# Kernel tuning notes

Measured on AMD Instinct MI355X. Metric: run time of the kernel, lower is better.

## Reference

```python
import jax, jax.numpy as jnp
import numpy as np


def setup_inputs() -> dict:
    key = jax.random.key(0)
    k1, k2, k3 = jax.random.split(key, 3)
    x = jax.random.normal(k1, (64, 64, 128, 128), dtype=jnp.float32)
    weight = jax.random.normal(k2, (256, 64, 3, 3), dtype=jnp.float32)
    bias = jax.random.normal(k3, (256,), dtype=jnp.float32)
    return {"x": x, "weight": weight, "bias": bias}


def reference(x, weight, bias):
    # Conv2d, stride 1, no padding (VALID), NCHW / OIHW layout
    y = jax.lax.conv_general_dilated(
        x, weight,
        window_strides=(1, 1),
        padding='VALID',
        dimension_numbers=('NCHW', 'OIHW', 'NCHW'),
    )
    y = y + bias[None, :, None, None]  # [B, C_out, H_out, W_out]
    # tanh-approximate GELU (matches the Triton kernel's formula)
    y = jax.nn.gelu(y, approximate=True)
    # global average pool over spatial dims -> [B, C_out]
    return jnp.mean(y, axis=(2, 3))
```

## Files before the change

kernel.cpp:

```cpp
#include <hip/hip_runtime.h>


typedef __attribute__((ext_vector_type(8))) short short8;
typedef __attribute__((ext_vector_type(4))) float floatx4;
typedef __attribute__((ext_vector_type(4))) unsigned int uintx4;
typedef __attribute__((ext_vector_type(2))) unsigned int uintx2;

#define HO 126
#define CIP 72

__device__ __forceinline__ unsigned int f2bf(float f) {
    unsigned int u = __float_as_uint(f);
    return (u + 0x7FFFu + ((u >> 16) & 1u)) >> 16;
}

__device__ __forceinline__ float gelu_t(float y) {
    float p = __builtin_fmaf(0.044715f, y * y, 1.0f);
    float z2 = -2.3022084f * y * p;
    float e = exp2f(z2);
    return y * __builtin_amdgcn_rcpf(1.0f + e);
}

__global__ __launch_bounds__(256)
void prep_kernel(const float* __restrict__ wgt, float* __restrict__ out,
                 unsigned short* __restrict__ wb2) {
    int g = blockIdx.x * 256 + threadIdx.x;
    if (g < 64 * 256) out[g] = 0.f;
    if (g < 147456) {
        int j    = g & 7;
        int lane = (g >> 3) & 63;
        int fc   = g >> 9;
        int cog  = fc & 15;
        int half = (fc >> 4) & 1;
        int tap  = fc >> 5;
        int li = lane & 15, quad = lane >> 4;
        int co = cog * 16 + li;
        int ci = half * 32 + quad * 8 + j;
        wb2[g] = (unsigned short)f2bf(wgt[(co * 64 + ci) * 9 + tap]);
    }
}

__global__ __launch_bounds__(512, 4)
void conv_kernel(const float* __restrict__ x, const float* __restrict__ bias,
                 const unsigned short* __restrict__ wb2, float* __restrict__ out) {
    __shared__ unsigned short xs[3][130][CIP];

    const int bx = blockIdx.x;
    const int n = bx / HO;
    const int h = bx % HO;
    const int tid  = threadIdx.x;
    const int lane = tid & 63;
    const int wave = tid >> 6;
    const int li   = lane & 15;
    const int quad = lane >> 4;
    const int sc = wave & 3;
    const int sp = wave >> 2;
    const int coBase  = sc * 64;
    const int pixBase = sp * 64;

    {
        const int col = tid & 127;
        const int g   = tid >> 7;
        const float* xg = x + (size_t)n * 64 * 16384 + h * 128 + col;
#pragma unroll
        for (int i = 0; i < 12; ++i) {
            int idx = g * 12 + i;
            int r  = idx >> 4;
            int cq = idx & 15;
            float v0 = xg[(size_t)(cq * 4 + 0) * 16384 + r * 128];
            float v1 = xg[(size_t)(cq * 4 + 1) * 16384 + r * 128];
            float v2 = xg[(size_t)(cq * 4 + 2) * 16384 + r * 128];
            float v3 = xg[(size_t)(cq * 4 + 3) * 16384 + r * 128];
            uintx2 pk;
            pk.x = f2bf(v0) | (f2bf(v1) << 16);
            pk.y = f2bf(v2) | (f2bf(v3) << 16);
            *reinterpret_cast<uintx2*>(&xs[r][col][cq * 4]) = pk;
        }
    }

    floatx4 acc[16];
#pragma unroll
    for (int i = 0; i < 16; ++i) acc[i] = (floatx4){0.f, 0.f, 0.f, 0.f};

    __syncthreads();

    union Frag { uintx4 u; short8 s; };
    const unsigned short* xbase = &xs[0][pixBase + li][0] + quad * 8;
    const unsigned short* abase = wb2 + (size_t)(sc * 4) * 512 + lane * 8;

#pragma unroll
    for (int tap = 0; tap < 9; ++tap) {
        const int kh = tap / 3;
        const int kw = tap % 3;
        Frag a[8];
#pragma unroll
        for (int hf = 0; hf < 2; ++hf)
#pragma unroll
            for (int cf = 0; cf < 4; ++cf)
                a[hf * 4 + cf].u = *reinterpret_cast<const uintx4*>(
                    abase + (size_t)(((tap * 2 + hf) * 16) + cf) * 512);
#pragma unroll
        for (int hf = 0; hf < 2; ++hf)
#pragma unroll
            for (int pf = 0; pf < 4; ++pf) {
                Frag b;
                b.u = *reinterpret_cast<const uintx4*>(
                    xbase + (kh * 130 + kw + pf * 16) * CIP + hf * 32);
#pragma unroll
                for (int cf = 0; cf < 4; ++cf)
                    acc[cf * 4 + pf] = __builtin_amdgcn_mfma_f32_16x16x32_bf16(
                        a[hf * 4 + cf].s, b.s, acc[cf * 4 + pf], 0, 0, 0);
            }
    }

    const float inv = 1.0f / (126.f * 126.f);
#pragma unroll
    for (int cf = 0; cf < 4; ++cf) {
        const floatx4 bv = *reinterpret_cast<const floatx4*>(
            bias + coBase + cf * 16 + quad * 4);
        floatx4 s = (floatx4){0.f, 0.f, 0.f, 0.f};
#pragma unroll
        for (int pf = 0; pf < 4; ++pf) {
            bool valid = (pixBase + pf * 16 + li) < 126;
#pragma unroll
            for (int r = 0; r < 4; ++r) {
                float gv = gelu_t(acc[cf * 4 + pf][r] + bv[r]);
                s[r] += valid ? gv : 0.f;
            }
        }
#pragma unroll
        for (int r = 0; r < 4; ++r) {
            float v = s[r];
            v += __shfl_xor(v, 1);
            v += __shfl_xor(v, 2);
            v += __shfl_xor(v, 4);
            v += __shfl_xor(v, 8);
            if (li == 0)
                atomicAdd(&out[n * 256 + coBase + cf * 16 + quad * 4 + r], v * inv);
        }
    }
}

extern "C" void kernel_launch(void* const* d_in, const int* in_sizes, int n_in,
                              void* d_out, int out_size, void* d_ws, size_t ws_size,
                              hipStream_t stream) {
    const float* x    = (const float*)d_in[0];
    const float* wgt  = (const float*)d_in[1];
    const float* bias = (const float*)d_in[2];
    float* out = (float*)d_out;
    unsigned short* wb2 = (unsigned short*)d_ws;

    prep_kernel<<<576, 256, 0, stream>>>(wgt, out, wb2);
    conv_kernel<<<64 * HO, 512, 0, stream>>>(x, bias, wb2, out);
}
```

Baseline: 681.7 us.

## Process nine output rows per block with rotating 4-row LDS ring and prefetch

```diff
diff --git a/kernel.cpp b/kernel.cpp
--- a/kernel.cpp
+++ b/kernel.cpp
@@ -4,10 +4,9 @@
 typedef __attribute__((ext_vector_type(8))) short short8;
 typedef __attribute__((ext_vector_type(4))) float floatx4;
 typedef __attribute__((ext_vector_type(4))) unsigned int uintx4;
-typedef __attribute__((ext_vector_type(2))) unsigned int uintx2;
 
-#define HO 126
-#define CIP 72
+#define NGRP 14
+#define LROWS 9
 
 __device__ __forceinline__ unsigned int f2bf(float f) {
     unsigned int u = __float_as_uint(f);
@@ -16,8 +15,7 @@
 
 __device__ __forceinline__ float gelu_t(float y) {
     float p = __builtin_fmaf(0.044715f, y * y, 1.0f);
-    float z2 = -2.3022084f * y * p;
-    float e = exp2f(z2);
+    float e = exp2f(-2.3022084f * y * p);
     return y * __builtin_amdgcn_rcpf(1.0f + e);
 }
 
@@ -43,11 +41,12 @@
 __global__ __launch_bounds__(512, 4)
 void conv_kernel(const float* __restrict__ x, const float* __restrict__ bias,
                  const unsigned short* __restrict__ wb2, float* __restrict__ out) {
-    __shared__ unsigned short xs[3][130][CIP];
+    __shared__ unsigned short xs[4][128][64];
+    unsigned short* xsf = &xs[0][0][0];
 
     const int bx = blockIdx.x;
-    const int n = bx / HO;
-    const int h = bx % HO;
+    const int n  = bx / NGRP;
+    const int R0 = (bx % NGRP) * LROWS;
     const int tid  = threadIdx.x;
     const int lane = tid & 63;
     const int wave = tid >> 6;
@@ -58,86 +57,122 @@
     const int coBase  = sc * 64;
     const int pixBase = sp * 64;
 
-    {
-        const int col = tid & 127;
-        const int g   = tid >> 7;
-        const float* xg = x + (size_t)n * 64 * 16384 + h * 128 + col;
+    const int col = tid & 127;
+    const int cig = tid >> 7;
+    const float* xg = x + (size_t)n * 64 * 16384 + (size_t)cig * 16 * 16384 + col;
+    const int w0 = col * 64 + (((cig * 2    ) + col) & 7) * 8;
+    const int w1 = col * 64 + (((cig * 2 + 1) + col) & 7) * 8;
+
+    int boff[3][2];
 #pragma unroll
-        for (int i = 0; i < 12; ++i) {
-            int idx = g * 12 + i;
-            int r  = idx >> 4;
-            int cq = idx & 15;
-            float v0 = xg[(size_t)(cq * 4 + 0) * 16384 + r * 128];
-            float v1 = xg[(size_t)(cq * 4 + 1) * 16384 + r * 128];
-            float v2 = xg[(size_t)(cq * 4 + 2) * 16384 + r * 128];
-            float v3 = xg[(size_t)(cq * 4 + 3) * 16384 + r * 128];
-            uintx2 pk;
-            pk.x = f2bf(v0) | (f2bf(v1) << 16);
-            pk.y = f2bf(v2) | (f2bf(v3) << 16);
-            *reinterpret_cast<uintx2*>(&xs[r][col][cq * 4]) = pk;
-        }
-    }
+    for (int kw = 0; kw < 3; ++kw)
+#pragma unroll
+        for (int hf = 0; hf < 2; ++hf)
+            boff[kw][hf] = (pixBase + li + kw) * 64
+                         + ((hf * 4 + quad + kw + li) & 7) * 8;
 
-    floatx4 acc[16];
-#pragma unroll
-    for (int i = 0; i < 16; ++i) acc[i] = (floatx4){0.f, 0.f, 0.f, 0.f};
-
-    __syncthreads();
-
-    union Frag { uintx4 u; short8 s; };
-    const unsigned short* xbase = &xs[0][pixBase + li][0] + quad * 8;
     const unsigned short* abase = wb2 + (size_t)(sc * 4) * 512 + lane * 8;
 
 #pragma unroll
-    for (int tap = 0; tap < 9; ++tap) {
-        const int kh = tap / 3;
-        const int kw = tap % 3;
-        Frag a[8];
+    for (int r = 0; r < 3; ++r) {
+        float v[16];
 #pragma unroll
-        for (int hf = 0; hf < 2; ++hf)
+        for (int k = 0; k < 16; ++k)
+            v[k] = xg[(size_t)(R0 + r) * 128 + (size_t)k * 16384];
+        uintx4 p0, p1;
 #pragma unroll
-            for (int cf = 0; cf < 4; ++cf)
-                a[hf * 4 + cf].u = *reinterpret_cast<const uintx4*>(
-                    abase + (size_t)(((tap * 2 + hf) * 16) + cf) * 512);
+        for (int j = 0; j < 4; ++j) {
+            p0[j] = f2bf(v[2*j])     | (f2bf(v[2*j+1]) << 16);
+            p1[j] = f2bf(v[8+2*j])   | (f2bf(v[9+2*j]) << 16);
+        }
+        *reinterpret_cast<uintx4*>(xsf + r * 8192 + w0) = p0;
+        *reinterpret_cast<uintx4*>(xsf + r * 8192 + w1) = p1;
+    }
+
+    int sA = 0, sB = 8192, sC = 16384, sD = 24576;
+    __syncthreads();
+
+    const float inv = 1.0f / (126.f * 126.f);
+    union Frag { uintx4 u; short8 s; };
+
+#pragma unroll 1
+    for (int h = 0; h < LROWS; ++h) {
+        float v[16];
+        const bool do_stage = (h < LROWS - 1);
+        if (do_stage) {
 #pragma unroll
-        for (int hf = 0; hf < 2; ++hf)
+            for (int k = 0; k < 16; ++k)
+                v[k] = xg[(size_t)(R0 + h + 3) * 128 + (size_t)k * 16384];
+        }
+
+        floatx4 acc[16];
+#pragma unroll
+        for (int i = 0; i < 16; ++i) acc[i] = (floatx4){0.f, 0.f, 0.f, 0.f};
+
+        const int sk[3] = { sA, sB, sC };
+#pragma unroll
+        for (int tap = 0; tap < 9; ++tap) {
+            const int kh = tap / 3, kw = tap % 3;
+            const int sb = sk[kh];
+#pragma unroll
+            for (int hf = 0; hf < 2; ++hf) {
+                Frag a[4];
+#pragma unroll
+                for (int cf = 0; cf < 4; ++cf)
+                    a[cf].u = *reinterpret_cast<const uintx4*>(
+                        abase + (size_t)(((tap * 2 + hf) * 16) + cf) * 512);
+#pragma unroll
+                for (int pf = 0; pf < 4; ++pf) {
+                    Frag b;
+                    b.u = *reinterpret_cast<const uintx4*>(
+                        xsf + sb + boff[kw][hf] + pf * 1024);
+#pragma unroll
+                    for (int cf = 0; cf < 4; ++cf)
+                        acc[cf * 4 + pf] = __builtin_amdgcn_mfma_f32_16x16x32_bf16(
+                            a[cf].s, b.s, acc[cf * 4 + pf], 0, 0, 0);
+                }
+            }
+        }
+
+        if (do_stage) {
+            uintx4 p0, p1;
+#pragma unroll
+            for (int j = 0; j < 4; ++j) {
+                p0[j] = f2bf(v[2*j])   | (f2bf(v[2*j+1]) << 16);
+                p1[j] = f2bf(v[8+2*j]) | (f2bf(v[9+2*j]) << 16);
+            }
+            *reinterpret_cast<uintx4*>(xsf + sD + w0) = p0;
+            *reinterpret_cast<uintx4*>(xsf + sD + w1) = p1;
+        }
+
+#pragma unroll
+        for (int cf = 0; cf < 4; ++cf) {
+            const floatx4 bv = *reinterpret_cast<const floatx4*>(
+                bias + coBase + cf * 16 + quad * 4);
+            floatx4 s = (floatx4){0.f, 0.f, 0.f, 0.f};
 #pragma unroll
             for (int pf = 0; pf < 4; ++pf) {
-                Frag b;
-                b.u = *reinterpret_cast<const uintx4*>(
-                    xbase + (kh * 130 + kw + pf * 16) * CIP + hf * 32);
+                bool valid = (pixBase + pf * 16 + li) < 126;
 #pragma unroll
-                for (int cf = 0; cf < 4; ++cf)
-                    acc[cf * 4 + pf] = __builtin_amdgcn_mfma_f32_16x16x32_bf16(
-                        a[hf * 4 + cf].s, b.s, acc[cf * 4 + pf], 0, 0, 0);
+                for (int r = 0; r < 4; ++r) {
+                    float gv = gelu_t(acc[cf * 4 + pf][r] + bv[r]);
+                    s[r] += valid ? gv : 0.f;
+                }
             }
-    }
-
-    const float inv = 1.0f / (126.f * 126.f);
-#pragma unroll
-    for (int cf = 0; cf < 4; ++cf) {
-        const floatx4 bv = *reinterpret_cast<const floatx4*>(
-            bias + coBase + cf * 16 + quad * 4);
-        floatx4 s = (floatx4){0.f, 0.f, 0.f, 0.f};
-#pragma unroll
-        for (int pf = 0; pf < 4; ++pf) {
-            bool valid = (pixBase + pf * 16 + li) < 126;
 #pragma unroll
             for (int r = 0; r < 4; ++r) {
-                float gv = gelu_t(acc[cf * 4 + pf][r] + bv[r]);
-                s[r] += valid ? gv : 0.f;
+                float vv = s[r];
+                vv += __shfl_xor(vv, 1);
+                vv += __shfl_xor(vv, 2);
+                vv += __shfl_xor(vv, 4);
+                vv += __shfl_xor(vv, 8);
+                if (li == 0)
+                    atomicAdd(&out[n * 256 + coBase + cf * 16 + quad * 4 + r], vv * inv);
             }
         }
-#pragma unroll
-        for (int r = 0; r < 4; ++r) {
-            float v = s[r];
-            v += __shfl_xor(v, 1);
-            v += __shfl_xor(v, 2);
-            v += __shfl_xor(v, 4);
-            v += __shfl_xor(v, 8);
-            if (li == 0)
-                atomicAdd(&out[n * 256 + coBase + cf * 16 + quad * 4 + r], v * inv);
-        }
+
+        __syncthreads();
+        int t = sA; sA = sB; sB = sC; sC = sD; sD = t;
     }
 }
 
@@ -151,5 +186,5 @@
     unsigned short* wb2 = (unsigned short*)d_ws;
 
     prep_kernel<<<576, 256, 0, stream>>>(wgt, out, wb2);
-    conv_kernel<<<64 * HO, 512, 0, stream>>>(x, bias, wb2, out);
+    conv_kernel<<<64 * NGRP, 512, 0, stream>>>(x, bias, wb2, out);
 }
```

New measurement: 1.617 ms. 2.37x slower.
